# Performance work log

Hardware: AMD Instinct MI355X
Metric: run time of the kernel (lower is better)

## Reference

```python
import jax, jax.numpy as jnp
import numpy as np

B = 8192        # batch
F = 16          # num_fields
V = 50000       # vocab per field
D = 32          # embed_dim (all equal per assert)
NE = 3          # number of embedding spaces
NL = 3          # cross-net layers
EOD = F * D     # 512 = embed_output_dim
M1, M2, M3 = 512, 256, 128
REG_WEIGHT = 0.01


def setup_inputs() -> dict:
    key = jax.random.key(0)
    ks = jax.random.split(key, 12)
    x = jax.random.randint(ks[0], (B, F), 0, V)
    emb_tables = jax.random.normal(ks[1], (NE, F * V, D), dtype=jnp.float32) * 0.05
    cross_W = jax.random.normal(ks[2], (NE, NL, EOD, EOD), dtype=jnp.float32) * (1.0 / np.sqrt(EOD))
    cross_b = jnp.zeros((NE, NL, EOD), dtype=jnp.float32)
    mlp1_W = jax.random.normal(ks[3], (NE, EOD, M1), dtype=jnp.float32) * (1.0 / np.sqrt(EOD))
    mlp1_b = jnp.zeros((NE, M1), dtype=jnp.float32)
    mlp_W1 = jax.random.normal(ks[4], (M1, M2), dtype=jnp.float32) * (1.0 / np.sqrt(M1))
    mlp_b1 = jnp.zeros((M2,), dtype=jnp.float32)
    mlp_W2 = jax.random.normal(ks[5], (M2, M3), dtype=jnp.float32) * (1.0 / np.sqrt(M2))
    mlp_b2 = jnp.zeros((M3,), dtype=jnp.float32)
    mlp_W3 = jax.random.normal(ks[6], (M3, 1), dtype=jnp.float32) * (1.0 / np.sqrt(M3))
    mlp_b3 = jnp.zeros((1,), dtype=jnp.float32)
    return {"x": x, "emb_tables": emb_tables, "cross_W": cross_W, "cross_b": cross_b,
            "mlp1_W": mlp1_W, "mlp1_b": mlp1_b, "mlp_W1": mlp_W1, "mlp_b1": mlp_b1,
            "mlp_W2": mlp_W2, "mlp_b2": mlp_b2, "mlp_W3": mlp_W3, "mlp_b3": mlp_b3}


def _branch(x0, Ws, bs, W1, b1):
    # DCNv2 cross network: x_{l+1} = x0 * (W_l x_l + b_l) + x_l, then one MLP layer (ReLU)
    xl = x0
    for l in range(NL):
        xl = x0 * (xl @ Ws[l] + bs[l]) + xl
    return jax.nn.relu(xl @ W1 + b1)


def reference(x, emb_tables, cross_W, cross_b, mlp1_W, mlp1_b,
              mlp_W1, mlp_b1, mlp_W2, mlp_b2, mlp_W3, mlp_b3):
    offsets = jnp.arange(F, dtype=x.dtype) * V
    idx = x + offsets                      # [B, F] indices into shared table
    es = emb_tables[:, idx]                # [NE, B, F, D]
    es_flat = es.reshape(NE, B, EOD)       # [NE, B, F*D]
    h = jax.vmap(_branch)(es_flat, cross_W, cross_b, mlp1_W, mlp1_b)  # [NE, B, M1]
    h = h.mean(axis=0)                     # mean over embedding spaces
    h = jax.nn.relu(h @ mlp_W1 + mlp_b1)
    h = jax.nn.relu(h @ mlp_W2 + mlp_b2)
    p = h @ mlp_W3 + mlp_b3                # [B, 1]
    output = jax.nn.sigmoid(p[:, 0])
    # training-path regularizer: per-field cross-embedding Gram SVDs
    pairs = [(1, 0), (2, 0), (2, 1)]
    sims = []
    for i, j in pairs:
        m = jnp.einsum('bkd,bke->kde', es[i], es[j])     # [F, D, D]
        s = jnp.linalg.svd(m, compute_uv=False)          # batched singular values [F, D]
        sims.append(s.mean(axis=0))                      # [D]
    sim = jnp.concatenate(sims)                          # [len(pairs)*D]
    reg_loss = REG_WEIGHT * jnp.mean(sim ** 2)
    return output, reg_loss
```

## Files before the change

### kernel.cpp

```cpp
#include <hip/hip_runtime.h>
#include <math.h>

#define B_ 8192
#define F_ 16
#define V_ 50000
#define D_ 32
#define NE_ 3
#define EOD_ 512
#define M1_ 512
#define M2_ 256
#define M3_ 128
#define BE_ ((size_t)B_ * EOD_)

typedef __attribute__((ext_vector_type(8))) short short8;
typedef __attribute__((ext_vector_type(4))) float floatx4;
typedef __attribute__((ext_vector_type(4))) unsigned short us4;

__device__ __forceinline__ unsigned short f2bf(float f) {
    union { float f; unsigned u; } v; v.f = f;
    unsigned r = v.u + 0x7FFF + ((v.u >> 16) & 1);
    return (unsigned short)(r >> 16);
}
__device__ __forceinline__ float bf2f(unsigned short h) {
    union { unsigned u; float f; } v; v.u = (unsigned)h << 16;
    return v.f;
}
__device__ __forceinline__ void gld16(const void* g, void* l) {
    __builtin_amdgcn_global_load_lds(
        (const __attribute__((address_space(1))) unsigned int*)g,
        (__attribute__((address_space(3))) unsigned int*)l, 16, 0, 0);
}
__device__ __forceinline__ void sum3st(const unsigned short* p, unsigned short* l) {
    uint4 a = *(const uint4*)p;
    uint4 b = *(const uint4*)(p + BE_);
    uint4 c = *(const uint4*)(p + 2 * BE_);
    const unsigned short* pa = (const unsigned short*)&a;
    const unsigned short* pb = (const unsigned short*)&b;
    const unsigned short* pc = (const unsigned short*)&c;
    unsigned short r[8];
    #pragma unroll
    for (int j = 0; j < 8; j++) r[j] = f2bf(bf2f(pa[j]) + bf2f(pb[j]) + bf2f(pc[j]));
    *(uint4*)l = *(uint4*)r;
}

__device__ __forceinline__ void wtrans_dev(const float* __restrict__ W,
    unsigned short* __restrict__ Wt, int K, int N, int bx, int by, int t,
    float (*tile)[33])
{
    int bn = bx * 32, bk = by * 32;
    int tx = t & 31, ty = t >> 5;
    #pragma unroll
    for (int i = 0; i < 32; i += 8)
        tile[ty + i][tx] = W[(size_t)(bk + ty + i) * N + bn + tx];
    __syncthreads();
    #pragma unroll
    for (int i = 0; i < 32; i += 8)
        Wt[(size_t)(bn + ty + i) * K + bk + tx] = f2bf(tile[tx][ty + i]);
}

__global__ __launch_bounds__(256) void prep_k(
    const int* __restrict__ x, const float* __restrict__ emb,
    const float* __restrict__ crossW, const float* __restrict__ mlp1W,
    const float* __restrict__ W1, const float* __restrict__ W2,
    unsigned short* __restrict__ WtC, unsigned short* __restrict__ Wt1,
    unsigned short* __restrict__ Wt2, unsigned short* __restrict__ esb,
    float* __restrict__ mbuf)
{
    __shared__ float tile[32][33];
    int blk = blockIdx.x;
    int t = threadIdx.x;
    if (blk < 3072) {
        int bx = blk & 15, by = (blk >> 4) & 15, mat = blk >> 8;
        const float* Wm = (mat < 9) ? crossW + (size_t)mat * 512 * 512
                                    : mlp1W + (size_t)(mat - 9) * 512 * 512;
        wtrans_dev(Wm, WtC + (size_t)mat * 512 * 512, 512, 512, bx, by, t, tile);
    } else if (blk < 3200) {
        int r = blk - 3072;
        wtrans_dev(W1, Wt1, 512, 256, r & 7, r >> 3, t, tile);
    } else if (blk < 3232) {
        int r = blk - 3200;
        wtrans_dev(W2, Wt2, 256, 128, r & 3, r >> 2, t, tile);
    } else if (blk < 9376) {
        int gid = (blk - 3232) * 256 + t;
        int d8 = gid & 3;
        int f  = (gid >> 2) & 15;
        int b  = (gid >> 6) & (B_ - 1);
        int e  = gid >> 19;
        int idx = x[b * F_ + f] + f * V_;
        const float4* src = (const float4*)(emb + ((size_t)e * F_ * V_ + idx) * D_) + d8 * 2;
        float4 v0 = src[0], v1 = src[1];
        unsigned short o[8];
        o[0] = f2bf(v0.x); o[1] = f2bf(v0.y); o[2] = f2bf(v0.z); o[3] = f2bf(v0.w);
        o[4] = f2bf(v1.x); o[5] = f2bf(v1.y); o[6] = f2bf(v1.z); o[7] = f2bf(v1.w);
        unsigned short* dst = esb + ((size_t)e * B_ + b) * EOD_ + f * D_ + d8 * 8;
        *(uint4*)dst = *(uint4*)o;
    } else {
        int r = blk - 9376;
        mbuf[(size_t)r * 256 + t] = 0.f;
    }
}

__device__ void pairsum_dev(const unsigned short* es, float* m, int ablk, int t,
                            void* smemv)
{
    const int pi[3] = {1, 2, 2};
    const int pj[3] = {0, 0, 1};
    int pk = ablk % 48, by = ablk / 48;
    int pair = pk >> 4, k = pk & 15;
    const unsigned short* Ei = es + (size_t)pi[pair] * BE_ + k * D_;
    const unsigned short* Ej = es + (size_t)pj[pair] * BE_ + k * D_;
    int b0 = by * (B_ / 16);

    float (*sa)[32] = (float(*)[32])smemv;
    float (*sb)[32] = sa + 8;
    int d = t >> 3, e4 = (t & 7) * 4;
    int lr = t >> 5, lc = t & 31;
    float a0 = 0, a1 = 0, a2 = 0, a3 = 0;

    for (int bb = b0; bb < b0 + B_ / 16; bb += 8) {
        __syncthreads();
        sa[lr][lc] = bf2f(Ei[(size_t)(bb + lr) * EOD_ + lc]);
        sb[lr][lc] = bf2f(Ej[(size_t)(bb + lr) * EOD_ + lc]);
        __syncthreads();
        #pragma unroll
        for (int s2 = 0; s2 < 8; s2++) {
            float avv = sa[s2][d];
            float4 bvv = *(const float4*)&sb[s2][e4];
            a0 += avv * bvv.x; a1 += avv * bvv.y;
            a2 += avv * bvv.z; a3 += avv * bvv.w;
        }
    }
    float* dst = m + (size_t)pk * 1024 + d * 32 + e4;
    atomicAdd(dst + 0, a0); atomicAdd(dst + 1, a1);
    atomicAdd(dst + 2, a2); atomicAdd(dst + 3, a3);
}

template<int PHASE>
__device__ void svd_dev(const float* mg, float* st, float* sv, int ablk, int t,
                        void* smemv)
{
    if (ablk >= 48 || t >= 64) return;
    int mat = ablk;
    int l = t;
    int col = l & 31, half = l >> 5;
    float a[16];
    if (PHASE == 0) {
        const float* src = mg + (size_t)mat * 1024 + half * 16 * 32 + col;
        #pragma unroll
        for (int j = 0; j < 16; j++) a[j] = src[j * 32];
    } else {
        #pragma unroll
        for (int j = 0; j < 16; j++) a[j] = st[(size_t)(mat * 16 + j) * 64 + l];
    }

    for (int sweep = 0; sweep < 3; sweep++) {
        for (int r = 0; r < 31; r++) {
            int partner, isp;
            if (col == 31) { partner = r; isp = 1; }
            else {
                int u = col - r; if (u < 0) u += 31;
                if (u == 0) { partner = 31; isp = 0; }
                else {
                    int v = 2 * r - col; v %= 31; if (v < 0) v += 31;
                    partner = v;
                    isp = (u <= 15) ? 1 : 0;
                }
            }
            int plane = half * 32 + partner;
            float b[16];
            #pragma unroll
            for (int j = 0; j < 16; j++) b[j] = __shfl(a[j], plane, 64);
            float own = 0.f, cross = 0.f, par = 0.f;
            #pragma unroll
            for (int j = 0; j < 16; j++) {
                own   += a[j] * a[j];
                cross += a[j] * b[j];
                par   += b[j] * b[j];
            }
            own   += __shfl_xor(own, 32);
            cross += __shfl_xor(cross, 32);
            par   += __shfl_xor(par, 32);
            float app = isp ? own : par;
            float aqq = isp ? par : own;
            float c = 1.f, s = 0.f;
            if (fabsf(cross) > 1e-12f) {
                float tau = (aqq - app) / (2.f * cross);
                float tt = (tau >= 0.f) ? 1.f / (tau + sqrtf(1.f + tau * tau))
                                        : 1.f / (tau - sqrtf(1.f + tau * tau));
                c = rsqrtf(1.f + tt * tt); s = tt * c;
            }
            float sgn = isp ? -s : s;
            #pragma unroll
            for (int j = 0; j < 16; j++) a[j] = c * a[j] + sgn * b[j];
        }
    }

    if (PHASE == 0) {
        #pragma unroll
        for (int j = 0; j < 16; j++) st[(size_t)(mat * 16 + j) * 64 + l] = a[j];
        return;
    }

    float nn = 0.f;
    #pragma unroll
    for (int j = 0; j < 16; j++) nn += a[j] * a[j];
    nn += __shfl_xor(nn, 32);
    float v = sqrtf(nn);

    float* ev = (float*)smemv;
    if (half == 0) ev[col] = v;
    if (half == 0) {
        int rank = 0;
        for (int o2 = 0; o2 < 32; o2++) {
            float w = ev[o2];
            if (w > v || (w == v && o2 < col)) rank++;
        }
        sv[(size_t)mat * 32 + rank] = v;
    }
}

__device__ void reg_dev(const float* sv, float* outf, int ablk, int t, void* smemv)
{
    if (ablk != 0) return;
    float* red = (float*)smemv;
    float val = 0.f;
    if (t < 96) {
        int p = t >> 5, d = t & 31;
        float s = 0;
        #pragma unroll
        for (int k = 0; k < 16; k++) s += sv[(size_t)(p * 16 + k) * 32 + d];
        s *= (1.f / 16.f);
        val = s * s;
    }
    red[t] = val; __syncthreads();
    for (int off = 128; off > 0; off >>= 1) {
        if (t < off) red[t] += red[t + off];
        __syncthreads();
    }
    if (t == 0) outf[B_] = 0.01f * red[0] / 96.f;
}

template<int MODE, int AUX, int ASUM>
__global__ __launch_bounds__(256) void gemm_k(
    const unsigned short* __restrict__ A,  long sA,
    const unsigned short* __restrict__ Wt, long sW,
    const float* __restrict__ bias,        long sB,
    const unsigned short* __restrict__ x0, long sX,
    const unsigned short* __restrict__ xl, long sXl,
    unsigned short* __restrict__ outb,     long sO,
    int M, int N, int K,
    const unsigned short* __restrict__ es, float* __restrict__ mbuf,
    float* __restrict__ svst, float* __restrict__ svb,
    const float* __restrict__ W3, const float* __restrict__ b3,
    float* __restrict__ outf)
{
    __shared__ __align__(16) unsigned char smem[32768];
    int t = threadIdx.x;

    if (AUX && blockIdx.z >= 3) {
        int ablk = (blockIdx.z - 3) * 256 + blockIdx.y * 4 + blockIdx.x;
        if (AUX == 1)      pairsum_dev(es, mbuf, ablk, t, smem);
        else if (AUX == 2) svd_dev<0>(mbuf, svst, svb, ablk, t, smem);
        else if (AUX == 3) svd_dev<1>(mbuf, svst, svb, ablk, t, smem);
        else               reg_dev(svb, outf, ablk, t, smem);
        return;
    }

    int e = blockIdx.z;
    A    += (size_t)e * sA;
    Wt   += (size_t)e * sW;
    bias += (size_t)e * sB;
    outb += (size_t)e * sO;
    if (MODE == 0) { x0 += (size_t)e * sX; xl += (size_t)e * sXl; }

    unsigned short* As = (unsigned short*)smem;
    unsigned short* Bs = As + 128 * 64;
    int w = t >> 6, lane = t & 63;
    int quad = lane >> 4, lid = lane & 15;
    int wr = (w & 1) * 64, wc = (w >> 1) * 64;
    int rowbase = blockIdx.y * 128, colbase = blockIdx.x * 128;

    int r4 = t >> 3;
    int c8 = (t & 7) * 8;
    const unsigned short* Ab = A  + (size_t)rowbase * K + c8;
    const unsigned short* Bb = Wt + (size_t)colbase * K + c8;
    unsigned short* lA = As + t * 8;
    unsigned short* lB = Bs + t * 8;

    floatx4 acc[4][4];
    #pragma unroll
    for (int i = 0; i < 4; i++)
        #pragma unroll
        for (int j = 0; j < 4; j++) acc[i][j] = {0.f, 0.f, 0.f, 0.f};

    for (int k0 = 0; k0 < K; k0 += 64) {
        if (k0) __syncthreads();
        #pragma unroll
        for (int i = 0; i < 4; i++) {
            size_t go = (size_t)(i * 32 + r4) * K + k0;
            if (ASUM) sum3st(Ab + go, lA + i * 2048);
            else      gld16(Ab + go, lA + i * 2048);
            gld16(Bb + go, lB + i * 2048);
        }
        __syncthreads();
        #pragma unroll
        for (int s = 0; s < 2; s++) {
            short8 af[4], bfr[4];
            #pragma unroll
            for (int i = 0; i < 4; i++) {
                af[i]  = *(const short8*)(As + (wr + i * 16 + lid) * 64 + s * 32 + quad * 8);
                bfr[i] = *(const short8*)(Bs + (wc + i * 16 + lid) * 64 + s * 32 + quad * 8);
            }
            #pragma unroll
            for (int i = 0; i < 4; i++)
                #pragma unroll
                for (int j = 0; j < 4; j++)
                    acc[i][j] = __builtin_amdgcn_mfma_f32_16x16x32_bf16(bfr[j], af[i], acc[i][j], 0, 0, 0);
        }
    }

    if (MODE == 3) {
        __syncthreads();
        unsigned short* h2s = (unsigned short*)smem;
        #pragma unroll
        for (int i = 0; i < 4; i++) {
            int rl = wr + i * 16 + lid;
            int sw = (rl & 7) << 3;
            #pragma unroll
            for (int j = 0; j < 4; j++) {
                int col0 = wc + j * 16 + quad * 4;
                float4 bv = *(const float4*)(bias + col0);
                float v0 = fmaxf(acc[i][j][0] + bv.x, 0.f);
                float v1 = fmaxf(acc[i][j][1] + bv.y, 0.f);
                float v2 = fmaxf(acc[i][j][2] + bv.z, 0.f);
                float v3 = fmaxf(acc[i][j][3] + bv.w, 0.f);
                us4 o = { f2bf(v0), f2bf(v1), f2bf(v2), f2bf(v3) };
                *(us4*)(h2s + (size_t)rl * 128 + (col0 ^ sw)) = o;
            }
        }
        __syncthreads();
        if (t < 128) {
            int sw = (t & 7) << 3;
            const unsigned short* hr = h2s + (size_t)t * 128;
            float p = 0.f;
            #pragma unroll
            for (int cc = 0; cc < 128; cc += 4) {
                us4 hv = *(const us4*)(hr + (cc ^ sw));
                float4 wv = *(const float4*)(W3 + cc);
                p += bf2f(hv.x) * wv.x + bf2f(hv.y) * wv.y
                   + bf2f(hv.z) * wv.z + bf2f(hv.w) * wv.w;
            }
            outf[rowbase + t] = 1.0f / (1.0f + expf(-(p + b3[0])));
        }
        return;
    }

    #pragma unroll
    for (int i = 0; i < 4; i++) {
        int row = rowbase + wr + i * 16 + lid;
        #pragma unroll
        for (int j = 0; j < 4; j++) {
            int col0 = colbase + wc + j * 16 + quad * 4;
            size_t off = (size_t)row * N + col0;
            float4 bv = *(const float4*)(bias + col0);
            float v0 = acc[i][j][0] + bv.x;
            float v1 = acc[i][j][1] + bv.y;
            float v2 = acc[i][j][2] + bv.z;
            float v3 = acc[i][j][3] + bv.w;
            if (MODE == 0) {
                us4 xv = *(const us4*)(x0 + off);
                us4 lv = *(const us4*)(xl + off);
                v0 = bf2f(xv.x) * v0 + bf2f(lv.x);
                v1 = bf2f(xv.y) * v1 + bf2f(lv.y);
                v2 = bf2f(xv.z) * v2 + bf2f(lv.z);
                v3 = bf2f(xv.w) * v3 + bf2f(lv.w);
            } else if (MODE == 1) {
                v0 = fmaxf(v0, 0.f) * (1.f / 3.f);
                v1 = fmaxf(v1, 0.f) * (1.f / 3.f);
                v2 = fmaxf(v2, 0.f) * (1.f / 3.f);
                v3 = fmaxf(v3, 0.f) * (1.f / 3.f);
            } else {
                v0 = fmaxf(v0, 0.f);
                v1 = fmaxf(v1, 0.f);
                v2 = fmaxf(v2, 0.f);
                v3 = fmaxf(v3, 0.f);
            }
            us4 o = { f2bf(v0), f2bf(v1), f2bf(v2), f2bf(v3) };
            *(us4*)(outb + off) = o;
        }
    }
}

extern "C" void kernel_launch(void* const* d_in, const int* in_sizes, int n_in,
                              void* d_out, int out_size, void* d_ws, size_t ws_size,
                              hipStream_t stream)
{
    const int*   x      = (const int*)d_in[0];
    const float* emb    = (const float*)d_in[1];
    const float* crossW = (const float*)d_in[2];
    const float* crossb = (const float*)d_in[3];
    const float* mlp1W  = (const float*)d_in[4];
    const float* mlp1b  = (const float*)d_in[5];
    const float* W1     = (const float*)d_in[6];
    const float* b1     = (const float*)d_in[7];
    const float* W2     = (const float*)d_in[8];
    const float* b2     = (const float*)d_in[9];
    const float* W3     = (const float*)d_in[10];
    const float* b3     = (const float*)d_in[11];
    float* out = (float*)d_out;

    unsigned char* wsb = (unsigned char*)d_ws;
    size_t o = 0;
    auto alloc = [&](size_t bytes) -> void* {
        void* p = wsb + o; o += (bytes + 255) & ~(size_t)255; return p;
    };
    unsigned short* esb  = (unsigned short*)alloc(3 * BE_ * 2);
    unsigned short* B0   = (unsigned short*)alloc(3 * BE_ * 2);
    unsigned short* B1   = (unsigned short*)alloc(3 * BE_ * 2);
    unsigned short* WtC  = (unsigned short*)alloc((size_t)12 * 512 * 512 * 2);
    unsigned short* Wt1  = (unsigned short*)alloc((size_t)512 * 256 * 2);
    unsigned short* Wt2  = (unsigned short*)alloc((size_t)256 * 128 * 2);
    float*          mbuf = (float*)alloc(48 * 1024 * 4);
    float*          svst = (float*)alloc(48 * 16 * 64 * 4);
    float*          svb  = (float*)alloc(48 * 32 * 4);
    unsigned short* WtM  = WtC + (size_t)9 * 512 * 512;
    unsigned short* h1b  = esb;

    prep_k<<<9568, 256, 0, stream>>>(x, emb, crossW, mlp1W, W1, W2,
                                     WtC, Wt1, Wt2, esb, mbuf);

    const long sW512 = 3 * 512 * 512;

    gemm_k<0, 1, 0><<<dim3(4, 64, 6), 256, 0, stream>>>(
        esb, (long)BE_, WtC, sW512, crossb, 3 * 512,
        esb, (long)BE_, esb, (long)BE_, B0, (long)BE_, B_, EOD_, EOD_,
        esb, mbuf, svst, svb, nullptr, nullptr, nullptr);
    gemm_k<0, 2, 0><<<dim3(4, 64, 4), 256, 0, stream>>>(
        B0, (long)BE_, WtC + 512 * 512, sW512, crossb + 512, 3 * 512,
        esb, (long)BE_, B0, (long)BE_, B1, (long)BE_, B_, EOD_, EOD_,
        nullptr, mbuf, svst, svb, nullptr, nullptr, nullptr);
    gemm_k<0, 3, 0><<<dim3(4, 64, 4), 256, 0, stream>>>(
        B1, (long)BE_, WtC + 2 * 512 * 512, sW512, crossb + 1024, 3 * 512,
        esb, (long)BE_, B1, (long)BE_, B0, (long)BE_, B_, EOD_, EOD_,
        nullptr, mbuf, svst, svb, nullptr, nullptr, nullptr);
    gemm_k<1, 4, 0><<<dim3(4, 64, 4), 256, 0, stream>>>(
        B0, (long)BE_, WtM, 512 * 512, mlp1b, 512,
        nullptr, 0, nullptr, 0, B1, (long)BE_, B_, M1_, EOD_,
        nullptr, mbuf, svst, svb, nullptr, nullptr, out);
    gemm_k<2, 0, 1><<<dim3(2, 64, 1), 256, 0, stream>>>(
        B1, 0, Wt1, 0, b1, 0, nullptr, 0, nullptr, 0,
        h1b, 0, B_, M2_, M1_,
        nullptr, nullptr, nullptr, nullptr, nullptr, nullptr, nullptr);
    gemm_k<3, 0, 0><<<dim3(1, 64, 1), 256, 0, stream>>>(
        h1b, 0, Wt2, 0, b2, 0, nullptr, 0, nullptr, 0,
        nullptr, 0, B_, M3_, M2_,
        nullptr, nullptr, nullptr, nullptr, W3, b3, out);
}
```

Before: 664.5 us.

## Fuse three cross layers and MLP1 into one LDS-resident kernel per tile

Replaces the four separate cross/MLP1 GEMM launches with a single fused kernel. Each block keeps a 32-row activation panel in double-buffered LDS and runs all three cross layers plus the first MLP layer. This removes the round trips of the intermediate B0/B1 activations through global memory and cuts launch count. The SVD singular-value reduction now goes through atomics plus a last-block-done counter instead of a separate reg pass, and the SVD work rides on the remaining MLP GEMM launches. In exchange, the small 32-row tiles reread all weights from global per block, and the 64KB LDS panel may limit occupancy.

```diff
diff --git a/kernel.cpp b/kernel.cpp
--- a/kernel.cpp
+++ b/kernel.cpp
@@ -64,7 +64,7 @@
     const float* __restrict__ W1, const float* __restrict__ W2,
     unsigned short* __restrict__ WtC, unsigned short* __restrict__ Wt1,
     unsigned short* __restrict__ Wt2, unsigned short* __restrict__ esb,
-    float* __restrict__ mbuf)
+    float* __restrict__ mbuf, float* __restrict__ psum)
 {
     __shared__ float tile[32][33];
     int blk = blockIdx.x;
@@ -94,9 +94,11 @@
         o[4] = f2bf(v1.x); o[5] = f2bf(v1.y); o[6] = f2bf(v1.z); o[7] = f2bf(v1.w);
         unsigned short* dst = esb + ((size_t)e * B_ + b) * EOD_ + f * D_ + d8 * 8;
         *(uint4*)dst = *(uint4*)o;
-    } else {
+    } else if (blk < 9568) {
         int r = blk - 9376;
         mbuf[(size_t)r * 256 + t] = 0.f;
+    } else {
+        if (t < 128) psum[t] = 0.f;
     }
 }
 
@@ -136,8 +138,8 @@
 }
 
 template<int PHASE>
-__device__ void svd_dev(const float* mg, float* st, float* sv, int ablk, int t,
-                        void* smemv)
+__device__ void svd_dev(const float* mg, float* st, float* psum, float* outf,
+                        int ablk, int t, void* smemv)
 {
     if (ablk >= 48 || t >= 64) return;
     int mat = ablk;
@@ -215,63 +217,160 @@
             float w = ev[o2];
             if (w > v || (w == v && o2 < col)) rank++;
         }
-        sv[(size_t)mat * 32 + rank] = v;
-    }
-}
-
-__device__ void reg_dev(const float* sv, float* outf, int ablk, int t, void* smemv)
-{
-    if (ablk != 0) return;
-    float* red = (float*)smemv;
-    float val = 0.f;
-    if (t < 96) {
-        int p = t >> 5, d = t & 31;
-        float s = 0;
-        #pragma unroll
-        for (int k = 0; k < 16; k++) s += sv[(size_t)(p * 16 + k) * 32 + d];
-        s *= (1.f / 16.f);
-        val = s * s;
-    }
-    red[t] = val; __syncthreads();
-    for (int off = 128; off > 0; off >>= 1) {
-        if (t < off) red[t] += red[t + off];
+        atomicAdd(&psum[(mat >> 4) * 32 + rank], v);
+    }
+    __threadfence();
+    unsigned old = 0;
+    if (t == 0) old = atomicAdd((unsigned*)(psum + 96), 1u);
+    old = (unsigned)__shfl((int)old, 0, 64);
+    if (old == 47u) {
+        float x1 = atomicAdd(&psum[t], 0.f);
+        float s1 = x1 * (1.f / 16.f);
+        float val = s1 * s1;
+        if (t < 32) {
+            float x2 = atomicAdd(&psum[64 + t], 0.f);
+            float s2 = x2 * (1.f / 16.f);
+            val += s2 * s2;
+        }
+        #pragma unroll
+        for (int off = 32; off > 0; off >>= 1) val += __shfl_down(val, off);
+        if (t == 0) outf[B_] = 0.01f * val / 96.f;
+    }
+}
+
+__device__ __forceinline__ void kloop512(const unsigned short* __restrict__ WtL,
+    const unsigned short* pan, int wc, int lid, int quad, floatx4 (&acc)[2][8])
+{
+    #pragma unroll
+    for (int i = 0; i < 2; i++)
+        #pragma unroll
+        for (int j = 0; j < 8; j++) acc[i][j] = {0.f, 0.f, 0.f, 0.f};
+    const unsigned char* pb = (const unsigned char*)pan;
+    int rsw = (lid & 7) << 4;
+    #pragma unroll 2
+    for (int k0 = 0; k0 < 512; k0 += 32) {
+        int kb = (k0 + quad * 8) * 2;
+        short8 a0 = *(const short8*)(pb + (lid << 10) + (kb ^ rsw));
+        short8 a1 = *(const short8*)(pb + ((16 + lid) << 10) + (kb ^ rsw));
+        #pragma unroll
+        for (int j = 0; j < 8; j++) {
+            short8 bfrag = *(const short8*)(WtL + (size_t)(wc + j * 16 + lid) * 512
+                                            + k0 + quad * 8);
+            acc[0][j] = __builtin_amdgcn_mfma_f32_16x16x32_bf16(bfrag, a0, acc[0][j], 0, 0, 0);
+            acc[1][j] = __builtin_amdgcn_mfma_f32_16x16x32_bf16(bfrag, a1, acc[1][j], 0, 0, 0);
+        }
+    }
+}
+
+__global__ __launch_bounds__(256, 2) void fused_k(
+    const unsigned short* __restrict__ esb,
+    const unsigned short* __restrict__ WtC,
+    const float* __restrict__ crossb,
+    const float* __restrict__ mlp1b,
+    unsigned short* __restrict__ B1,
+    float* __restrict__ mbuf)
+{
+    __shared__ __align__(16) unsigned short panel[2][32 * 512];
+    int t = threadIdx.x;
+    int blk = blockIdx.x;
+    if (blk >= 768) { pairsum_dev(esb, mbuf, blk - 768, t, (void*)panel); return; }
+    int e = blk >> 8, p = blk & 255;
+    int w = t >> 6, lane = t & 63, quad = lane >> 4, lid = lane & 15;
+    int wc = w * 128;
+    const unsigned short* esP = esb + ((size_t)e * B_ + (size_t)p * 32) * 512;
+
+    #pragma unroll
+    for (int rnd = 0; rnd < 8; rnd++) {
+        int L = rnd * 4096 + t * 16;
+        int sw = ((L >> 10) & 7) << 4;
+        gld16((const unsigned char*)esP + (L ^ sw),
+              (unsigned char*)panel[0] + rnd * 4096 + w * 1024);
+    }
+
+    us4 x0r[2][8];
+    #pragma unroll
+    for (int i = 0; i < 2; i++)
+        #pragma unroll
+        for (int j = 0; j < 8; j++)
+            x0r[i][j] = *(const us4*)(esP + (size_t)(i * 16 + lid) * 512
+                                      + wc + j * 16 + quad * 4);
+    __syncthreads();
+
+    floatx4 acc[2][8];
+    int cur = 0;
+    #pragma unroll 1
+    for (int l = 0; l < 3; l++) {
+        const unsigned short* WtL = WtC + (size_t)(e * 3 + l) * 262144;
+        kloop512(WtL, panel[cur], wc, lid, quad, acc);
+        const float* bias = crossb + (e * 3 + l) * 512;
+        const unsigned char* pold = (const unsigned char*)panel[cur];
+        unsigned char* pnew = (unsigned char*)panel[cur ^ 1];
+        #pragma unroll
+        for (int i = 0; i < 2; i++) {
+            int row = i * 16 + lid;
+            int rsw = (row & 7) << 4;
+            #pragma unroll
+            for (int j = 0; j < 8; j++) {
+                int col = wc + j * 16 + quad * 4;
+                int boff = (row << 10) + ((col << 1) ^ rsw);
+                float4 bv = *(const float4*)(bias + col);
+                us4 xlv = *(const us4*)(pold + boff);
+                us4 xv = x0r[i][j];
+                float v0 = bf2f(xv.x) * (acc[i][j][0] + bv.x) + bf2f(xlv.x);
+                float v1 = bf2f(xv.y) * (acc[i][j][1] + bv.y) + bf2f(xlv.y);
+                float v2 = bf2f(xv.z) * (acc[i][j][2] + bv.z) + bf2f(xlv.z);
+                float v3 = bf2f(xv.w) * (acc[i][j][3] + bv.w) + bf2f(xlv.w);
+                us4 o = { f2bf(v0), f2bf(v1), f2bf(v2), f2bf(v3) };
+                *(us4*)(pnew + boff) = o;
+            }
+        }
         __syncthreads();
-    }
-    if (t == 0) outf[B_] = 0.01f * red[0] / 96.f;
-}
-
-template<int MODE, int AUX, int ASUM>
+        cur ^= 1;
+    }
+    {
+        const unsigned short* WtL = WtC + (size_t)(9 + e) * 262144;
+        kloop512(WtL, panel[cur], wc, lid, quad, acc);
+        const float* bias = mlp1b + e * 512;
+        unsigned short* outp = B1 + ((size_t)e * B_ + (size_t)p * 32) * 512;
+        #pragma unroll
+        for (int i = 0; i < 2; i++) {
+            int row = i * 16 + lid;
+            #pragma unroll
+            for (int j = 0; j < 8; j++) {
+                int col = wc + j * 16 + quad * 4;
+                float4 bv = *(const float4*)(bias + col);
+                float v0 = fmaxf(acc[i][j][0] + bv.x, 0.f) * (1.f / 3.f);
+                float v1 = fmaxf(acc[i][j][1] + bv.y, 0.f) * (1.f / 3.f);
+                float v2 = fmaxf(acc[i][j][2] + bv.z, 0.f) * (1.f / 3.f);
+                float v3 = fmaxf(acc[i][j][3] + bv.w, 0.f) * (1.f / 3.f);
+                us4 o = { f2bf(v0), f2bf(v1), f2bf(v2), f2bf(v3) };
+                *(us4*)(outp + (size_t)row * 512 + col) = o;
+            }
+        }
+    }
+}
+
+template<int MODE, int AUX, int ASUM, int NZ>
 __global__ __launch_bounds__(256) void gemm_k(
-    const unsigned short* __restrict__ A,  long sA,
-    const unsigned short* __restrict__ Wt, long sW,
-    const float* __restrict__ bias,        long sB,
-    const unsigned short* __restrict__ x0, long sX,
-    const unsigned short* __restrict__ xl, long sXl,
-    unsigned short* __restrict__ outb,     long sO,
+    const unsigned short* __restrict__ A,
+    const unsigned short* __restrict__ Wt,
+    const float* __restrict__ bias,
+    unsigned short* __restrict__ outb,
     int M, int N, int K,
-    const unsigned short* __restrict__ es, float* __restrict__ mbuf,
-    float* __restrict__ svst, float* __restrict__ svb,
+    float* __restrict__ mbuf, float* __restrict__ svst, float* __restrict__ psum,
     const float* __restrict__ W3, const float* __restrict__ b3,
     float* __restrict__ outf)
 {
     __shared__ __align__(16) unsigned char smem[32768];
     int t = threadIdx.x;
 
-    if (AUX && blockIdx.z >= 3) {
-        int ablk = (blockIdx.z - 3) * 256 + blockIdx.y * 4 + blockIdx.x;
-        if (AUX == 1)      pairsum_dev(es, mbuf, ablk, t, smem);
-        else if (AUX == 2) svd_dev<0>(mbuf, svst, svb, ablk, t, smem);
-        else if (AUX == 3) svd_dev<1>(mbuf, svst, svb, ablk, t, smem);
-        else               reg_dev(svb, outf, ablk, t, smem);
+    if (AUX && (int)blockIdx.z >= NZ) {
+        int ablk = ((int)blockIdx.z - NZ) * (int)(gridDim.x * gridDim.y)
+                 + (int)blockIdx.y * (int)gridDim.x + (int)blockIdx.x;
+        if (AUX == 2) svd_dev<0>(mbuf, svst, psum, outf, ablk, t, smem);
+        else          svd_dev<1>(mbuf, svst, psum, outf, ablk, t, smem);
         return;
     }
-
-    int e = blockIdx.z;
-    A    += (size_t)e * sA;
-    Wt   += (size_t)e * sW;
-    bias += (size_t)e * sB;
-    outb += (size_t)e * sO;
-    if (MODE == 0) { x0 += (size_t)e * sX; xl += (size_t)e * sXl; }
 
     unsigned short* As = (unsigned short*)smem;
     unsigned short* Bs = As + 128 * 64;
@@ -342,15 +441,15 @@
         if (t < 128) {
             int sw = (t & 7) << 3;
             const unsigned short* hr = h2s + (size_t)t * 128;
-            float p = 0.f;
+            float pacc = 0.f;
             #pragma unroll
             for (int cc = 0; cc < 128; cc += 4) {
                 us4 hv = *(const us4*)(hr + (cc ^ sw));
                 float4 wv = *(const float4*)(W3 + cc);
-                p += bf2f(hv.x) * wv.x + bf2f(hv.y) * wv.y
-                   + bf2f(hv.z) * wv.z + bf2f(hv.w) * wv.w;
-            }
-            outf[rowbase + t] = 1.0f / (1.0f + expf(-(p + b3[0])));
+                pacc += bf2f(hv.x) * wv.x + bf2f(hv.y) * wv.y
+                      + bf2f(hv.z) * wv.z + bf2f(hv.w) * wv.w;
+            }
+            outf[rowbase + t] = 1.0f / (1.0f + expf(-(pacc + b3[0])));
         }
         return;
     }
@@ -363,28 +462,10 @@
             int col0 = colbase + wc + j * 16 + quad * 4;
             size_t off = (size_t)row * N + col0;
             float4 bv = *(const float4*)(bias + col0);
-            float v0 = acc[i][j][0] + bv.x;
-            float v1 = acc[i][j][1] + bv.y;
-            float v2 = acc[i][j][2] + bv.z;
-            float v3 = acc[i][j][3] + bv.w;
-            if (MODE == 0) {
-                us4 xv = *(const us4*)(x0 + off);
-                us4 lv = *(const us4*)(xl + off);
-                v0 = bf2f(xv.x) * v0 + bf2f(lv.x);
-                v1 = bf2f(xv.y) * v1 + bf2f(lv.y);
-                v2 = bf2f(xv.z) * v2 + bf2f(lv.z);
-                v3 = bf2f(xv.w) * v3 + bf2f(lv.w);
-            } else if (MODE == 1) {
-                v0 = fmaxf(v0, 0.f) * (1.f / 3.f);
-                v1 = fmaxf(v1, 0.f) * (1.f / 3.f);
-                v2 = fmaxf(v2, 0.f) * (1.f / 3.f);
-                v3 = fmaxf(v3, 0.f) * (1.f / 3.f);
-            } else {
-                v0 = fmaxf(v0, 0.f);
-                v1 = fmaxf(v1, 0.f);
-                v2 = fmaxf(v2, 0.f);
-                v3 = fmaxf(v3, 0.f);
-            }
+            float v0 = fmaxf(acc[i][j][0] + bv.x, 0.f);
+            float v1 = fmaxf(acc[i][j][1] + bv.y, 0.f);
+            float v2 = fmaxf(acc[i][j][2] + bv.z, 0.f);
+            float v3 = fmaxf(acc[i][j][3] + bv.w, 0.f);
             us4 o = { f2bf(v0), f2bf(v1), f2bf(v2), f2bf(v3) };
             *(us4*)(outb + off) = o;
         }
@@ -415,44 +496,24 @@
         void* p = wsb + o; o += (bytes + 255) & ~(size_t)255; return p;
     };
     unsigned short* esb  = (unsigned short*)alloc(3 * BE_ * 2);
-    unsigned short* B0   = (unsigned short*)alloc(3 * BE_ * 2);
-    unsigned short* B1   = (unsigned short*)alloc(3 * BE_ * 2);
+    unsigned short* B1b  = (unsigned short*)alloc(3 * BE_ * 2);
     unsigned short* WtC  = (unsigned short*)alloc((size_t)12 * 512 * 512 * 2);
     unsigned short* Wt1  = (unsigned short*)alloc((size_t)512 * 256 * 2);
     unsigned short* Wt2  = (unsigned short*)alloc((size_t)256 * 128 * 2);
     float*          mbuf = (float*)alloc(48 * 1024 * 4);
     float*          svst = (float*)alloc(48 * 16 * 64 * 4);
-    float*          svb  = (float*)alloc(48 * 32 * 4);
-    unsigned short* WtM  = WtC + (size_t)9 * 512 * 512;
+    float*          psum = (float*)alloc(128 * 4);
     unsigned short* h1b  = esb;
 
-    prep_k<<<9568, 256, 0, stream>>>(x, emb, crossW, mlp1W, W1, W2,
-                                     WtC, Wt1, Wt2, esb, mbuf);
-
-    const long sW512 = 3 * 512 * 512;
-
-    gemm_k<0, 1, 0><<<dim3(4, 64, 6), 256, 0, stream>>>(
-        esb, (long)BE_, WtC, sW512, crossb, 3 * 512,
-        esb, (long)BE_, esb, (long)BE_, B0, (long)BE_, B_, EOD_, EOD_,
-        esb, mbuf, svst, svb, nullptr, nullptr, nullptr);
-    gemm_k<0, 2, 0><<<dim3(4, 64, 4), 256, 0, stream>>>(
-        B0, (long)BE_, WtC + 512 * 512, sW512, crossb + 512, 3 * 512,
-        esb, (long)BE_, B0, (long)BE_, B1, (long)BE_, B_, EOD_, EOD_,
-        nullptr, mbuf, svst, svb, nullptr, nullptr, nullptr);
-    gemm_k<0, 3, 0><<<dim3(4, 64, 4), 256, 0, stream>>>(
-        B1, (long)BE_, WtC + 2 * 512 * 512, sW512, crossb + 1024, 3 * 512,
-        esb, (long)BE_, B1, (long)BE_, B0, (long)BE_, B_, EOD_, EOD_,
-        nullptr, mbuf, svst, svb, nullptr, nullptr, nullptr);
-    gemm_k<1, 4, 0><<<dim3(4, 64, 4), 256, 0, stream>>>(
-        B0, (long)BE_, WtM, 512 * 512, mlp1b, 512,
-        nullptr, 0, nullptr, 0, B1, (long)BE_, B_, M1_, EOD_,
-        nullptr, mbuf, svst, svb, nullptr, nullptr, out);
-    gemm_k<2, 0, 1><<<dim3(2, 64, 1), 256, 0, stream>>>(
-        B1, 0, Wt1, 0, b1, 0, nullptr, 0, nullptr, 0,
-        h1b, 0, B_, M2_, M1_,
-        nullptr, nullptr, nullptr, nullptr, nullptr, nullptr, nullptr);
-    gemm_k<3, 0, 0><<<dim3(1, 64, 1), 256, 0, stream>>>(
-        h1b, 0, Wt2, 0, b2, 0, nullptr, 0, nullptr, 0,
-        nullptr, 0, B_, M3_, M2_,
-        nullptr, nullptr, nullptr, nullptr, W3, b3, out);
-}
+    prep_k<<<9569, 256, 0, stream>>>(x, emb, crossW, mlp1W, W1, W2,
+                                     WtC, Wt1, Wt2, esb, mbuf, psum);
+
+    fused_k<<<1536, 256, 0, stream>>>(esb, WtC, crossb, mlp1b, B1b, mbuf);
+
+    gemm_k<2, 2, 1, 1><<<dim3(2, 64, 2), 256, 0, stream>>>(
+        B1b, Wt1, b1, h1b, B_, M2_, M1_,
+        mbuf, svst, psum, nullptr, nullptr, nullptr);
+    gemm_k<3, 3, 0, 1><<<dim3(1, 64, 2), 256, 0, stream>>>(
+        h1b, Wt2, b2, nullptr, B_, M3_, M2_,
+        mbuf, svst, psum, W3, b3, out);
+}
```

Measured after the change: 720.3 us. +8.4%, slower.
